# Optimization experiments

Measured on AMD Instinct MI355X. Metric: run time of the kernel, lower is better.

The kernel has to match this reference:

```python
import jax, jax.numpy as jnp
import numpy as np

ROPE_THETA = 10000.0


def apply_rope(q, k, cos, sin):
    # q,k: [B,H,S,D]; cos,sin: [S,D/2] -> broadcast [1,1,S,D/2]
    def rot(t):
        t2 = t.reshape(*t.shape[:-1], -1, 2)  # [B,H,S,D/2,2]
        te, to = t2[..., 0], t2[..., 1]
        c = cos[None, None, :, :]
        s = sin[None, None, :, :]
        re = te * c - to * s
        im = te * s + to * c
        return jnp.stack([re, im], axis=-1).reshape(t.shape)
    return rot(q), rot(k)


def setup_inputs() -> dict:
    key = jax.random.key(0)
    ks = jax.random.split(key, 4)
    B, S, D, H = 2, 2048, 1024, 16
    hd = D // H
    x = jax.random.normal(ks[0], (B, S, D), dtype=jnp.float32)
    # causal boolean mask (True = keep)
    mask = jnp.tril(jnp.ones((S, S), dtype=bool))[None, None]
    # rotary tables
    inv_freq = 1.0 / (ROPE_THETA ** (jnp.arange(0, hd, 2, dtype=jnp.float32) / hd))  # [hd/2]
    t = jnp.arange(S, dtype=jnp.float32)
    ang = t[:, None] * inv_freq[None, :]  # [S, hd/2]
    freqs_cos = jnp.cos(ang)
    freqs_sin = jnp.sin(ang)
    W_qkv = jax.random.normal(ks[1], (D, 3 * D), dtype=jnp.float32) * 0.02
    b_qkv = jnp.zeros((3 * D,), dtype=jnp.float32)
    W_o = jax.random.normal(ks[2], (D, D), dtype=jnp.float32) * 0.02
    b_o = jnp.zeros((D,), dtype=jnp.float32)
    return {"x": x, "mask": mask, "freqs_cos": freqs_cos, "freqs_sin": freqs_sin,
            "W_qkv": W_qkv, "b_qkv": b_qkv, "W_o": W_o, "b_o": b_o}


def reference(x, mask, freqs_cos, freqs_sin, W_qkv, b_qkv, W_o, b_o):
    B, S, D = x.shape
    H = 16
    hd = D // H
    scale = hd ** -0.5
    qkv = x @ W_qkv + b_qkv  # [B,S,3D]
    q, k, v = jnp.split(qkv, 3, axis=-1)
    q = q.reshape(B, S, H, hd).transpose(0, 2, 1, 3)  # [B,H,S,hd]
    k = k.reshape(B, S, H, hd).transpose(0, 2, 1, 3)
    v = v.reshape(B, S, H, hd).transpose(0, 2, 1, 3)
    q, k = apply_rope(q, k, freqs_cos, freqs_sin)
    scores = jnp.einsum('bhqd,bhkd->bhqk', q, k) * scale
    scores = jnp.where(mask, scores, jnp.finfo(scores.dtype).min)
    attn = jax.nn.softmax(scores, axis=-1)
    out = jnp.einsum('bhqk,bhkd->bhqd', attn, v)
    out = out.transpose(0, 2, 1, 3).reshape(B, S, D)
    return out @ W_o + b_o
```

## Files before the change

### kernel.cpp

```cpp
#include <hip/hip_runtime.h>
#include <hip/hip_bf16.h>
#include <stdint.h>

typedef unsigned short u16;
typedef __attribute__((ext_vector_type(8))) __bf16 bf16x8;
typedef __attribute__((ext_vector_type(4))) float f32x4;
typedef __attribute__((ext_vector_type(16))) float f32x16;
typedef __attribute__((ext_vector_type(8))) u16 u16x8;

__device__ __forceinline__ u16 f2bf(float f) {
  union { float f; unsigned int u; } v; v.f = f;
  unsigned int r = v.u + 0x7fffu + ((v.u >> 16) & 1u);
  return (u16)(r >> 16);
}
__device__ __forceinline__ unsigned pack2(float lo, float hi) {
  return (unsigned)f2bf(lo) | ((unsigned)f2bf(hi) << 16);
}

__device__ __forceinline__ f32x4 mfma16(bf16x8 a, bf16x8 b, f32x4 c) {
  return __builtin_amdgcn_mfma_f32_16x16x32_bf16(a, b, c, 0, 0, 0);
}
__device__ __forceinline__ f32x16 mfma32(bf16x8 a, bf16x8 b, f32x16 c) {
  return __builtin_amdgcn_mfma_f32_32x32x16_bf16(a, b, c, 0, 0, 0);
}

__device__ __forceinline__ void gload16(const void* g, void* l) {
  __builtin_amdgcn_global_load_lds((const __attribute__((address_space(1))) void*)g,
                                   (__attribute__((address_space(3))) void*)l,
                                   16, 0, 0);
}

__global__ void cast_bf16_kernel(const float* __restrict__ in, u16* __restrict__ out, int n) {
  int i = (blockIdx.x * 256 + threadIdx.x) * 8;
  if (i >= n) return;
  const float4* p = (const float4*)(in + i);
  float4 a = p[0], b = p[1];
  u16x8 o;
  o[0] = f2bf(a.x); o[1] = f2bf(a.y); o[2] = f2bf(a.z); o[3] = f2bf(a.w);
  o[4] = f2bf(b.x); o[5] = f2bf(b.y); o[6] = f2bf(b.z); o[7] = f2bf(b.w);
  *(u16x8*)(out + i) = o;
}

__global__ void transpose_cast_k(const float* __restrict__ in, u16* __restrict__ out,
                                 int R, int Ccols) {
  __shared__ float tile[64][65];
  const int c0 = (int)blockIdx.x << 6, r0 = (int)blockIdx.y << 6;
  const int tx = threadIdx.x & 63, ty = threadIdx.x >> 6;
#pragma unroll
  for (int i = ty; i < 64; i += 4)
    tile[i][tx] = in[(size_t)(r0 + i) * Ccols + c0 + tx];
  __syncthreads();
#pragma unroll
  for (int i = ty; i < 64; i += 4)
    out[(size_t)(c0 + i) * R + r0 + tx] = f2bf(tile[tx][i]);
}

__global__ __launch_bounds__(256, 2)
void gemm_qkv(const u16* __restrict__ A, const u16* __restrict__ Bt,
              const float* __restrict__ bias,
              const float* __restrict__ fc, const float* __restrict__ fs,
              u16* __restrict__ qr, u16* __restrict__ kr, u16* __restrict__ vr) {
  const int K = 1024;
  __shared__ __align__(16) u16 smem[128 * 136];
  u16* const As = smem;
  u16* const Bs = smem + 128 * 32;
  const int m0 = (int)(blockIdx.x / 24) << 7;
  const int n0 = (int)(blockIdx.x % 24) << 7;
  const int tid = threadIdx.x;
  const int l = tid & 63, lg = l >> 4, ll = l & 15;
  const int w = tid >> 6;
  const int wr = (w >> 1) << 6, wc = (w & 1) << 6;
  const int srow = tid >> 2, scol = (tid & 3) << 3;
  const u16* ga = A + (size_t)(m0 + srow) * K + scol;
  const u16* gb = Bt + (size_t)(n0 + srow) * K + scol;
  u16* la0 = &As[srow * 32 + scol];
  u16* la1 = &As[(srow + 64) * 32 + scol];
  u16* lb0 = &Bs[srow * 32 + scol];
  u16* lb1 = &Bs[(srow + 64) * 32 + scol];
  const size_t K64 = (size_t)64 * K;
  f32x4 acc[4][4] = {};
  for (int kt = 0; kt < K; kt += 32) {
    gload16(ga + kt, la0);
    gload16(ga + kt + K64, la1);
    gload16(gb + kt, lb0);
    gload16(gb + kt + K64, lb1);
    __syncthreads();
    bf16x8 a[4], b[4];
#pragma unroll
    for (int i = 0; i < 4; ++i) {
      a[i] = *(const bf16x8*)&As[(wr + i * 16 + ll) * 32 + lg * 8];
      b[i] = *(const bf16x8*)&Bs[(wc + i * 16 + ll) * 32 + lg * 8];
    }
#pragma unroll
    for (int mi = 0; mi < 4; ++mi)
#pragma unroll
      for (int ni = 0; ni < 4; ++ni)
        acc[mi][ni] = mfma16(a[mi], b[ni], acc[mi][ni]);
    __syncthreads();
  }
  const int sec = n0 >> 10;
  u16* const dst = (sec == 0) ? qr : (sec == 1) ? kr : vr;
  const int h0 = (n0 & 1023) >> 6;
#pragma unroll
  for (int ni = 0; ni < 4; ++ni) {
    const int cc = wc + ni * 16 + ll;
    const int n = n0 + cc;
    const int d = n & 63;
    const float bi_ = bias[n];
    const int i2 = d >> 1;
    const bool odd = d & 1;
#pragma unroll
    for (int mi = 0; mi < 4; ++mi) {
#pragma unroll
      for (int r = 0; r < 4; ++r) {
        const int rr = wr + mi * 16 + lg * 4 + r;
        const int s = (m0 + rr) & 2047;
        float v = acc[mi][ni][r] + bi_;
        if (sec < 2) {
          const float c = fc[s * 32 + i2], sn = fs[s * 32 + i2];
          const float p = __shfl_xor(v, 1);
          v = odd ? (p * sn + v * c) : (v * c - p * sn);
          if (sec == 0) v *= 0.125f;
        }
        smem[rr * 136 + cc] = f2bf(v);
      }
    }
  }
  __syncthreads();
#pragma unroll
  for (int it = 0; it < 8; ++it) {
    const int c = it * 256 + tid;
    const int j = c & 7, hh = (c >> 3) & 1, rr = c >> 4;
    const int row = m0 + rr;
    const int bb = row >> 11, ss = row & 2047;
    const uint4 val = *(const uint4*)&smem[rr * 136 + hh * 64 + j * 8];
    *(uint4*)&dst[((size_t)(((bb << 4) + h0 + hh) << 11) + ss) * 64 + j * 8] = val;
  }
}

__global__ __launch_bounds__(256, 2)
void gemm_bt(const u16* __restrict__ A, const u16* __restrict__ Bt,
             const float* __restrict__ bias, float* __restrict__ C,
             int M, int N, int K) {
  __shared__ u16 As[128 * 32];
  __shared__ u16 Bs[128 * 32];
  const int nb = N >> 7;
  const int m0 = (int)(blockIdx.x / nb) << 7;
  const int n0 = (int)(blockIdx.x % nb) << 7;
  const int tid = threadIdx.x;
  const int l = tid & 63, lg = l >> 4, ll = l & 15;
  const int w = tid >> 6;
  const int wr = (w >> 1) << 6, wc = (w & 1) << 6;
  const int srow = tid >> 2, scol = (tid & 3) << 3;
  const u16* ga = A + (size_t)(m0 + srow) * K + scol;
  const u16* gb = Bt + (size_t)(n0 + srow) * K + scol;
  u16* la0 = &As[srow * 32 + scol];
  u16* la1 = &As[(srow + 64) * 32 + scol];
  u16* lb0 = &Bs[srow * 32 + scol];
  u16* lb1 = &Bs[(srow + 64) * 32 + scol];
  const size_t K64 = (size_t)64 * K;
  f32x4 acc[4][4] = {};
  for (int kt = 0; kt < K; kt += 32) {
    gload16(ga + kt, la0);
    gload16(ga + kt + K64, la1);
    gload16(gb + kt, lb0);
    gload16(gb + kt + K64, lb1);
    __syncthreads();
    bf16x8 a[4], b[4];
#pragma unroll
    for (int i = 0; i < 4; ++i) {
      a[i] = *(const bf16x8*)&As[(wr + i * 16 + ll) * 32 + lg * 8];
      b[i] = *(const bf16x8*)&Bs[(wc + i * 16 + ll) * 32 + lg * 8];
    }
#pragma unroll
    for (int mi = 0; mi < 4; ++mi)
#pragma unroll
      for (int ni = 0; ni < 4; ++ni)
        acc[mi][ni] = mfma16(a[mi], b[ni], acc[mi][ni]);
    __syncthreads();
  }
#pragma unroll
  for (int mi = 0; mi < 4; ++mi) {
#pragma unroll
    for (int r = 0; r < 4; ++r) {
      const int row = m0 + wr + mi * 16 + lg * 4 + r;
      float* crow = C + (size_t)row * N + n0 + wc;
#pragma unroll
      for (int ni = 0; ni < 4; ++ni)
        crow[ni * 16 + ll] = acc[mi][ni][r] + bias[n0 + wc + ni * 16 + ll];
    }
  }
}

__global__ void v_transpose_bf16(const u16* __restrict__ vr, u16* __restrict__ vt) {
  __shared__ u16 tile[64][66];
  const int bh = blockIdx.x;
  const int s0 = (int)blockIdx.y << 6;
  const int tx = threadIdx.x & 63, ty = threadIdx.x >> 6;
#pragma unroll
  for (int i = ty; i < 64; i += 4)
    tile[i][tx] = vr[((size_t)bh * 2048 + s0 + i) * 64 + tx];
  __syncthreads();
#pragma unroll
  for (int i = ty; i < 64; i += 4)
    vt[((size_t)bh * 64 + i) * 2048 + s0 + tx] = tile[tx][i];
}

__global__ __launch_bounds__(256, 2)
void attn_k(const u16* __restrict__ qr, const u16* __restrict__ kr,
            const u16* __restrict__ vt, u16* __restrict__ aout) {
  __shared__ __align__(16) char kvlds[16384];
  const int bi = (int)blockIdx.x;
  const int bh = bi & 31;
  const int qt = (bi < 256) ? (15 - (bi >> 5)) : ((bi - 256) >> 5);
  const int tid = threadIdx.x;
  const int w = tid >> 6, l = tid & 63, hi = l >> 5, ql = l & 31;
  const u16* Q  = qr + (size_t)bh * (2048 * 64);
  const u16* Kp = kr + (size_t)bh * (2048 * 64);
  const u16* Vp = vt + (size_t)bh * (64 * 2048);
  const int q0w = (qt << 7) + (w << 5);
  const int qg = q0w + ql;
  bf16x8 qf[4];
#pragma unroll
  for (int mi = 0; mi < 4; ++mi)
    qf[mi] = *(const bf16x8*)&Q[(size_t)qg * 64 + mi * 16 + hi * 8];
  const int sr = tid >> 2, sc = (tid & 3) * 32;
  const int wo0 = (sr * 128 + sc) ^ ((sr & 7) << 4);
  const int wo1 = (sr * 128 + sc + 16) ^ ((sr & 7) << 4);
  const char* kga = (const char*)(Kp + (size_t)sr * 64) + sc;
  const char* vga = (const char*)(Vp + (size_t)sr * 2048) + sc;
  const int swz = (ql & 7) << 4;
  f32x16 oa = {}, ob = {};
  float mrow = -1e30f, lp = 0.f;
  const int nch = 2 * qt + 2;
  uint4 sk0 = *(const uint4*)(kga), sk1 = *(const uint4*)(kga + 16);
  uint4 sv0 = *(const uint4*)(vga), sv1 = *(const uint4*)(vga + 16);
  for (int ch = 0; ch < nch; ++ch) {
    asm volatile("s_waitcnt vmcnt(0)" ::: "memory");
    asm volatile("s_barrier" ::: "memory");
    *(uint4*)(kvlds + wo0) = sk0;
    *(uint4*)(kvlds + wo1) = sk1;
    *(uint4*)(kvlds + 8192 + wo0) = sv0;
    *(uint4*)(kvlds + 8192 + wo1) = sv1;
    if (ch + 1 < nch) {
      const size_t kof = (size_t)(ch + 1) * 8192;
      const size_t vof = (size_t)(ch + 1) * 128;
      sk0 = *(const uint4*)(kga + kof); sk1 = *(const uint4*)(kga + kof + 16);
      sv0 = *(const uint4*)(vga + vof); sv1 = *(const uint4*)(vga + vof + 16);
    }
    asm volatile("s_waitcnt lgkmcnt(0)" ::: "memory");
    asm volatile("s_barrier" ::: "memory");
    const int kb = ch << 6;
    if (kb > q0w + 31) continue;
    f32x16 s0 = {}, s1 = {};
#pragma unroll
    for (int mi = 0; mi < 4; ++mi) {
      const int cb = mi * 32 + hi * 16;
      const bf16x8 k0 = *(const bf16x8*)(kvlds + ((ql * 128 + cb) ^ swz));
      const bf16x8 k1 = *(const bf16x8*)(kvlds + (((32 + ql) * 128 + cb) ^ swz));
      s0 = mfma32(k0, qf[mi], s0);
      s1 = mfma32(k1, qf[mi], s1);
    }
    if (kb + 63 > q0w) {
#pragma unroll
      for (int r = 0; r < 16; ++r) {
        const int kvo = (r & 3) + 8 * (r >> 2) + 4 * hi;
        if (kb + kvo > qg) s0[r] = -1e30f;
        if (kb + 32 + kvo > qg) s1[r] = -1e30f;
      }
    }
    float mx = s0[0];
#pragma unroll
    for (int r = 1; r < 16; ++r) mx = fmaxf(mx, s0[r]);
#pragma unroll
    for (int r = 0; r < 16; ++r) mx = fmaxf(mx, s1[r]);
    mx = fmaxf(mx, __shfl_xor(mx, 32));
    if (!__all(mx <= mrow + 8.f)) {
      const float mn = fmaxf(mrow, mx);
      const float esc = __expf(mrow - mn);
      mrow = mn;
      lp *= esc;
#pragma unroll
      for (int r = 0; r < 16; ++r) { oa[r] *= esc; ob[r] *= esc; }
    }
    float p0[16], p1[16];
#pragma unroll
    for (int r = 0; r < 16; ++r) {
      p0[r] = __expf(s0[r] - mrow);
      p1[r] = __expf(s1[r] - mrow);
      lp += p0[r] + p1[r];
    }
    bf16x8 pb[4];
#pragma unroll
    for (int s = 0; s < 2; ++s) {
      const float* ps = s ? p1 : p0;
#pragma unroll
      for (int j = 0; j < 2; ++j) {
        const unsigned X0 = pack2(ps[j * 8 + 0], ps[j * 8 + 1]);
        const unsigned X1 = pack2(ps[j * 8 + 2], ps[j * 8 + 3]);
        const unsigned Y0 = pack2(ps[j * 8 + 4], ps[j * 8 + 5]);
        const unsigned Y1 = pack2(ps[j * 8 + 6], ps[j * 8 + 7]);
        const unsigned sX0 = (unsigned)__shfl_xor((int)X0, 32);
        const unsigned sX1 = (unsigned)__shfl_xor((int)X1, 32);
        const unsigned sY0 = (unsigned)__shfl_xor((int)Y0, 32);
        const unsigned sY1 = (unsigned)__shfl_xor((int)Y1, 32);
        union { unsigned u[4]; bf16x8 v; } t;
        t.u[0] = hi ? sY0 : X0;
        t.u[1] = hi ? sY1 : X1;
        t.u[2] = hi ? Y0 : sX0;
        t.u[3] = hi ? Y1 : sX1;
        pb[s * 2 + j] = t.v;
      }
    }
#pragma unroll
    for (int jj = 0; jj < 4; ++jj) {
      const int cb = jj * 32 + hi * 16;
      const bf16x8 va = *(const bf16x8*)(kvlds + 8192 + ((ql * 128 + cb) ^ swz));
      const bf16x8 vb = *(const bf16x8*)(kvlds + 8192 + (((32 + ql) * 128 + cb) ^ swz));
      oa = mfma32(va, pb[jj], oa);
      ob = mfma32(vb, pb[jj], ob);
    }
  }
  lp += __shfl_xor(lp, 32);
  const float inv = 1.0f / lp;
  const int hcol = (bh & 15) << 6;
  const int tok = ((bh >> 4) << 11) + qg;
  unsigned* orow = (unsigned*)(aout + (size_t)tok * 1024 + hcol);
#pragma unroll
  for (int r = 0; r < 16; r += 2) {
    const int d0 = (r & 3) + 8 * (r >> 2) + 4 * hi;
    orow[d0 >> 1]        = pack2(oa[r] * inv, oa[r + 1] * inv);
    orow[(32 + d0) >> 1] = pack2(ob[r] * inv, ob[r + 1] * inv);
  }
}

extern "C" void kernel_launch(void* const* d_in, const int* in_sizes, int n_in,
                              void* d_out, int out_size, void* d_ws, size_t ws_size,
                              hipStream_t stream) {
  const float* x    = (const float*)d_in[0];
  const float* fc   = (const float*)d_in[2];
  const float* fs   = (const float*)d_in[3];
  const float* Wqkv = (const float*)d_in[4];
  const float* bqkv = (const float*)d_in[5];
  const float* Wo   = (const float*)d_in[6];
  const float* bo   = (const float*)d_in[7];
  float* out = (float*)d_out;

  size_t off = 0;
  auto alloc = [&](size_t bytes) {
    void* p = (char*)d_ws + off;
    off += (bytes + 255) & ~(size_t)255;
    return p;
  };
  u16*   xb   = (u16*)  alloc(4096ull * 1024 * 2);
  u16*   wqt  = (u16*)  alloc(3072ull * 1024 * 2);
  u16*   wot  = (u16*)  alloc(1024ull * 1024 * 2);
  u16*   qr_  = (u16*)  alloc(32ull * 2048 * 64 * 2);
  u16*   kr_  = (u16*)  alloc(32ull * 2048 * 64 * 2);
  u16*   vr_  = (u16*)  alloc(32ull * 2048 * 64 * 2);
  u16*   vt_  = (u16*)  alloc(32ull * 64 * 2048 * 2);
  u16*   ao_  = (u16*)  alloc(4096ull * 1024 * 2);

  cast_bf16_kernel<<<2048, 256, 0, stream>>>(x, xb, 4096 * 1024);
  transpose_cast_k<<<dim3(48, 16), 256, 0, stream>>>(Wqkv, wqt, 1024, 3072);
  transpose_cast_k<<<dim3(16, 16), 256, 0, stream>>>(Wo, wot, 1024, 1024);
  gemm_qkv<<<dim3(32 * 24), 256, 0, stream>>>(xb, wqt, bqkv, fc, fs, qr_, kr_, vr_);
  v_transpose_bf16<<<dim3(32, 32), 256, 0, stream>>>(vr_, vt_);
  attn_k<<<dim3(512), 256, 0, stream>>>(qr_, kr_, vt_, ao_);
  gemm_bt<<<dim3(32 * 8), 256, 0, stream>>>(ao_, wot, bo, out, 4096, 1024, 1024);
}
```

Measured before the change: 140.5 us.

## Double K-step in GEMMs and load K/V straight into registers in attention

Both GEMM kernels now stage 64-wide K slices per barrier pair instead of 32, halving the number of syncs per tile. The attention kernel drops its shared-memory K/V staging and barriers. Each wave reads its K and V fragments directly from global memory, skips the upper 32-key half when it is fully masked, and raises wave priority around the MFMA blocks. The trade-off is more redundant global/L2 traffic, since each wave reloads K/V that were previously shared across the four waves, and the loads can no longer be prefetched ahead of compute.

```diff
diff --git a/kernel.cpp b/kernel.cpp
--- a/kernel.cpp
+++ b/kernel.cpp
@@ -63,7 +63,7 @@
   const int K = 1024;
   __shared__ __align__(16) u16 smem[128 * 136];
   u16* const As = smem;
-  u16* const Bs = smem + 128 * 32;
+  u16* const Bs = smem + 8192;
   const int m0 = (int)(blockIdx.x / 24) << 7;
   const int n0 = (int)(blockIdx.x % 24) << 7;
   const int tid = threadIdx.x;
@@ -73,29 +73,36 @@
   const int srow = tid >> 2, scol = (tid & 3) << 3;
   const u16* ga = A + (size_t)(m0 + srow) * K + scol;
   const u16* gb = Bt + (size_t)(n0 + srow) * K + scol;
-  u16* la0 = &As[srow * 32 + scol];
-  u16* la1 = &As[(srow + 64) * 32 + scol];
-  u16* lb0 = &Bs[srow * 32 + scol];
-  u16* lb1 = &Bs[(srow + 64) * 32 + scol];
   const size_t K64 = (size_t)64 * K;
+  u16* const la00 = &As[srow * 32 + scol];
+  u16* const la01 = &As[4096 + srow * 32 + scol];
+  u16* const la10 = &As[(srow + 64) * 32 + scol];
+  u16* const la11 = &As[4096 + (srow + 64) * 32 + scol];
+  u16* const lb00 = &Bs[srow * 32 + scol];
+  u16* const lb01 = &Bs[4096 + srow * 32 + scol];
+  u16* const lb10 = &Bs[(srow + 64) * 32 + scol];
+  u16* const lb11 = &Bs[4096 + (srow + 64) * 32 + scol];
   f32x4 acc[4][4] = {};
-  for (int kt = 0; kt < K; kt += 32) {
-    gload16(ga + kt, la0);
-    gload16(ga + kt + K64, la1);
-    gload16(gb + kt, lb0);
-    gload16(gb + kt + K64, lb1);
+  for (int kt = 0; kt < K; kt += 64) {
+    gload16(ga + kt, la00);       gload16(ga + kt + 32, la01);
+    gload16(ga + kt + K64, la10); gload16(ga + kt + K64 + 32, la11);
+    gload16(gb + kt, lb00);       gload16(gb + kt + 32, lb01);
+    gload16(gb + kt + K64, lb10); gload16(gb + kt + K64 + 32, lb11);
     __syncthreads();
-    bf16x8 a[4], b[4];
-#pragma unroll
-    for (int i = 0; i < 4; ++i) {
-      a[i] = *(const bf16x8*)&As[(wr + i * 16 + ll) * 32 + lg * 8];
-      b[i] = *(const bf16x8*)&Bs[(wc + i * 16 + ll) * 32 + lg * 8];
-    }
-#pragma unroll
-    for (int mi = 0; mi < 4; ++mi)
-#pragma unroll
-      for (int ni = 0; ni < 4; ++ni)
-        acc[mi][ni] = mfma16(a[mi], b[ni], acc[mi][ni]);
+#pragma unroll
+    for (int h = 0; h < 2; ++h) {
+      bf16x8 a[4], b[4];
+#pragma unroll
+      for (int i = 0; i < 4; ++i) {
+        a[i] = *(const bf16x8*)&As[h * 4096 + (wr + i * 16 + ll) * 32 + lg * 8];
+        b[i] = *(const bf16x8*)&Bs[h * 4096 + (wc + i * 16 + ll) * 32 + lg * 8];
+      }
+#pragma unroll
+      for (int mi = 0; mi < 4; ++mi)
+#pragma unroll
+        for (int ni = 0; ni < 4; ++ni)
+          acc[mi][ni] = mfma16(a[mi], b[ni], acc[mi][ni]);
+    }
     __syncthreads();
   }
   const int sec = n0 >> 10;
@@ -142,8 +149,8 @@
 void gemm_bt(const u16* __restrict__ A, const u16* __restrict__ Bt,
              const float* __restrict__ bias, float* __restrict__ C,
              int M, int N, int K) {
-  __shared__ u16 As[128 * 32];
-  __shared__ u16 Bs[128 * 32];
+  __shared__ __align__(16) u16 As[2 * 128 * 32];
+  __shared__ __align__(16) u16 Bs[2 * 128 * 32];
   const int nb = N >> 7;
   const int m0 = (int)(blockIdx.x / nb) << 7;
   const int n0 = (int)(blockIdx.x % nb) << 7;
@@ -154,29 +161,36 @@
   const int srow = tid >> 2, scol = (tid & 3) << 3;
   const u16* ga = A + (size_t)(m0 + srow) * K + scol;
   const u16* gb = Bt + (size_t)(n0 + srow) * K + scol;
-  u16* la0 = &As[srow * 32 + scol];
-  u16* la1 = &As[(srow + 64) * 32 + scol];
-  u16* lb0 = &Bs[srow * 32 + scol];
-  u16* lb1 = &Bs[(srow + 64) * 32 + scol];
   const size_t K64 = (size_t)64 * K;
+  u16* const la00 = &As[srow * 32 + scol];
+  u16* const la01 = &As[4096 + srow * 32 + scol];
+  u16* const la10 = &As[(srow + 64) * 32 + scol];
+  u16* const la11 = &As[4096 + (srow + 64) * 32 + scol];
+  u16* const lb00 = &Bs[srow * 32 + scol];
+  u16* const lb01 = &Bs[4096 + srow * 32 + scol];
+  u16* const lb10 = &Bs[(srow + 64) * 32 + scol];
+  u16* const lb11 = &Bs[4096 + (srow + 64) * 32 + scol];
   f32x4 acc[4][4] = {};
-  for (int kt = 0; kt < K; kt += 32) {
-    gload16(ga + kt, la0);
-    gload16(ga + kt + K64, la1);
-    gload16(gb + kt, lb0);
-    gload16(gb + kt + K64, lb1);
+  for (int kt = 0; kt < K; kt += 64) {
+    gload16(ga + kt, la00);       gload16(ga + kt + 32, la01);
+    gload16(ga + kt + K64, la10); gload16(ga + kt + K64 + 32, la11);
+    gload16(gb + kt, lb00);       gload16(gb + kt + 32, lb01);
+    gload16(gb + kt + K64, lb10); gload16(gb + kt + K64 + 32, lb11);
     __syncthreads();
-    bf16x8 a[4], b[4];
-#pragma unroll
-    for (int i = 0; i < 4; ++i) {
-      a[i] = *(const bf16x8*)&As[(wr + i * 16 + ll) * 32 + lg * 8];
-      b[i] = *(const bf16x8*)&Bs[(wc + i * 16 + ll) * 32 + lg * 8];
-    }
-#pragma unroll
-    for (int mi = 0; mi < 4; ++mi)
-#pragma unroll
-      for (int ni = 0; ni < 4; ++ni)
-        acc[mi][ni] = mfma16(a[mi], b[ni], acc[mi][ni]);
+#pragma unroll
+    for (int h = 0; h < 2; ++h) {
+      bf16x8 a[4], b[4];
+#pragma unroll
+      for (int i = 0; i < 4; ++i) {
+        a[i] = *(const bf16x8*)&As[h * 4096 + (wr + i * 16 + ll) * 32 + lg * 8];
+        b[i] = *(const bf16x8*)&Bs[h * 4096 + (wc + i * 16 + ll) * 32 + lg * 8];
+      }
+#pragma unroll
+      for (int mi = 0; mi < 4; ++mi)
+#pragma unroll
+        for (int ni = 0; ni < 4; ++ni)
+          acc[mi][ni] = mfma16(a[mi], b[ni], acc[mi][ni]);
+    }
     __syncthreads();
   }
 #pragma unroll
@@ -209,7 +223,6 @@
 __global__ __launch_bounds__(256, 2)
 void attn_k(const u16* __restrict__ qr, const u16* __restrict__ kr,
             const u16* __restrict__ vt, u16* __restrict__ aout) {
-  __shared__ __align__(16) char kvlds[16384];
   const int bi = (int)blockIdx.x;
   const int bh = bi & 31;
   const int qt = (bi < 256) ? (15 - (bi >> 5)) : ((bi - 256) >> 5);
@@ -224,43 +237,40 @@
 #pragma unroll
   for (int mi = 0; mi < 4; ++mi)
     qf[mi] = *(const bf16x8*)&Q[(size_t)qg * 64 + mi * 16 + hi * 8];
-  const int sr = tid >> 2, sc = (tid & 3) * 32;
-  const int wo0 = (sr * 128 + sc) ^ ((sr & 7) << 4);
-  const int wo1 = (sr * 128 + sc + 16) ^ ((sr & 7) << 4);
-  const char* kga = (const char*)(Kp + (size_t)sr * 64) + sc;
-  const char* vga = (const char*)(Vp + (size_t)sr * 2048) + sc;
-  const int swz = (ql & 7) << 4;
   f32x16 oa = {}, ob = {};
   float mrow = -1e30f, lp = 0.f;
-  const int nch = 2 * qt + 2;
-  uint4 sk0 = *(const uint4*)(kga), sk1 = *(const uint4*)(kga + 16);
-  uint4 sv0 = *(const uint4*)(vga), sv1 = *(const uint4*)(vga + 16);
-  for (int ch = 0; ch < nch; ++ch) {
-    asm volatile("s_waitcnt vmcnt(0)" ::: "memory");
-    asm volatile("s_barrier" ::: "memory");
-    *(uint4*)(kvlds + wo0) = sk0;
-    *(uint4*)(kvlds + wo1) = sk1;
-    *(uint4*)(kvlds + 8192 + wo0) = sv0;
-    *(uint4*)(kvlds + 8192 + wo1) = sv1;
-    if (ch + 1 < nch) {
-      const size_t kof = (size_t)(ch + 1) * 8192;
-      const size_t vof = (size_t)(ch + 1) * 128;
-      sk0 = *(const uint4*)(kga + kof); sk1 = *(const uint4*)(kga + kof + 16);
-      sv0 = *(const uint4*)(vga + vof); sv1 = *(const uint4*)(vga + vof + 16);
-    }
-    asm volatile("s_waitcnt lgkmcnt(0)" ::: "memory");
-    asm volatile("s_barrier" ::: "memory");
+  const int nchw = ((q0w + 31) >> 6) + 1;
+  for (int ch = 0; ch < nchw; ++ch) {
     const int kb = ch << 6;
-    if (kb > q0w + 31) continue;
+    const bool dohi = (kb + 32) <= (q0w + 31);
+    const u16* krow0 = Kp + (size_t)(kb + ql) * 64 + hi * 8;
+    const u16* krow1 = krow0 + 32 * 64;
+    bf16x8 kf0[4], kf1[4];
+#pragma unroll
+    for (int mi = 0; mi < 4; ++mi) kf0[mi] = *(const bf16x8*)(krow0 + mi * 16);
+    if (dohi) {
+#pragma unroll
+      for (int mi = 0; mi < 4; ++mi) kf1[mi] = *(const bf16x8*)(krow1 + mi * 16);
+    }
+    const int njj = dohi ? 4 : 2;
+    const u16* vrow0 = Vp + (size_t)ql * 2048 + kb + hi * 8;
+    const u16* vrow1 = vrow0 + 32 * 2048;
+    bf16x8 va[4], vb[4];
+#pragma unroll
+    for (int jj = 0; jj < 4; ++jj) {
+      if (jj >= njj) break;
+      va[jj] = *(const bf16x8*)(vrow0 + jj * 16);
+      vb[jj] = *(const bf16x8*)(vrow1 + jj * 16);
+    }
     f32x16 s0 = {}, s1 = {};
-#pragma unroll
-    for (int mi = 0; mi < 4; ++mi) {
-      const int cb = mi * 32 + hi * 16;
-      const bf16x8 k0 = *(const bf16x8*)(kvlds + ((ql * 128 + cb) ^ swz));
-      const bf16x8 k1 = *(const bf16x8*)(kvlds + (((32 + ql) * 128 + cb) ^ swz));
-      s0 = mfma32(k0, qf[mi], s0);
-      s1 = mfma32(k1, qf[mi], s1);
-    }
+    __builtin_amdgcn_s_setprio(1);
+#pragma unroll
+    for (int mi = 0; mi < 4; ++mi) s0 = mfma32(kf0[mi], qf[mi], s0);
+    if (dohi) {
+#pragma unroll
+      for (int mi = 0; mi < 4; ++mi) s1 = mfma32(kf1[mi], qf[mi], s1);
+    }
+    __builtin_amdgcn_s_setprio(0);
     if (kb + 63 > q0w) {
 #pragma unroll
       for (int r = 0; r < 16; ++r) {
@@ -272,8 +282,10 @@
     float mx = s0[0];
 #pragma unroll
     for (int r = 1; r < 16; ++r) mx = fmaxf(mx, s0[r]);
-#pragma unroll
-    for (int r = 0; r < 16; ++r) mx = fmaxf(mx, s1[r]);
+    if (dohi) {
+#pragma unroll
+      for (int r = 0; r < 16; ++r) mx = fmaxf(mx, s1[r]);
+    }
     mx = fmaxf(mx, __shfl_xor(mx, 32));
     if (!__all(mx <= mrow + 8.f)) {
       const float mn = fmaxf(mrow, mx);
@@ -287,12 +299,20 @@
 #pragma unroll
     for (int r = 0; r < 16; ++r) {
       p0[r] = __expf(s0[r] - mrow);
-      p1[r] = __expf(s1[r] - mrow);
-      lp += p0[r] + p1[r];
+      lp += p0[r];
+    }
+    if (dohi) {
+#pragma unroll
+      for (int r = 0; r < 16; ++r) {
+        p1[r] = __expf(s1[r] - mrow);
+        lp += p1[r];
+      }
     }
     bf16x8 pb[4];
+    const int nseg = dohi ? 2 : 1;
 #pragma unroll
     for (int s = 0; s < 2; ++s) {
+      if (s >= nseg) break;
       const float* ps = s ? p1 : p0;
 #pragma unroll
       for (int j = 0; j < 2; ++j) {
@@ -312,14 +332,14 @@
         pb[s * 2 + j] = t.v;
       }
     }
+    __builtin_amdgcn_s_setprio(1);
 #pragma unroll
     for (int jj = 0; jj < 4; ++jj) {
-      const int cb = jj * 32 + hi * 16;
-      const bf16x8 va = *(const bf16x8*)(kvlds + 8192 + ((ql * 128 + cb) ^ swz));
-      const bf16x8 vb = *(const bf16x8*)(kvlds + 8192 + (((32 + ql) * 128 + cb) ^ swz));
-      oa = mfma32(va, pb[jj], oa);
-      ob = mfma32(vb, pb[jj], ob);
-    }
+      if (jj >= njj) break;
+      oa = mfma32(va[jj], pb[jj], oa);
+      ob = mfma32(vb[jj], pb[jj], ob);
+    }
+    __builtin_amdgcn_s_setprio(0);
   }
   lp += __shfl_xor(lp, 32);
   const float inv = 1.0f / lp;
```

After: 152.1 us. 1.08x slower.
